# Kernel tuning notes

Measured on AMD Instinct MI355X. Metric: run time of the kernel, lower is better.

Reference implementation:

```python
import jax, jax.numpy as jnp
import numpy as np

DIM = 2560; HEADS = 20; HEAD_DIM = 128
N_EXP = 4; TOP_K = 2; HID = 6912; SHID = 3584
B = 1; S = 2048
EPS = 1e-6


def setup_inputs():
    key = jax.random.key(0)
    ks = jax.random.split(key, 16)
    r = lambda i, shape, s=0.02: jax.random.normal(ks[i], shape, jnp.float32) * s
    # rope as [1,S,1,HD/2,2,2] rotation matrices: [[cos,-sin],[sin,cos]]
    ang = jax.random.uniform(ks[0], (1, S, 1, HEAD_DIM // 2), jnp.float32) * (2.0 * np.pi)
    c, s_ = jnp.cos(ang), jnp.sin(ang)
    rope = jnp.stack([jnp.stack([c, -s_], -1), jnp.stack([s_, c], -1)], -2)
    return dict(
        hidden_states=jax.random.normal(ks[1], (B, S, DIM), jnp.float32),
        temb=jax.random.normal(ks[2], (B, DIM), jnp.float32),
        rope=rope,
        adaln_w=r(3, (6 * DIM, DIM)), adaln_b=jnp.zeros((6 * DIM,), jnp.float32),
        qkv_w=r(4, (3 * DIM, DIM)), qkv_b=jnp.zeros((3 * DIM,), jnp.float32),
        qn_w=jnp.ones((DIM,), jnp.float32), kn_w=jnp.ones((DIM,), jnp.float32),
        out_w=r(5, (DIM, DIM)), out_b=jnp.zeros((DIM,), jnp.float32),
        gate_w=r(6, (N_EXP, DIM), 1.0 / DIM ** 0.5),
        ew1=r(7, (N_EXP, HID, DIM)), ew2=r(8, (N_EXP, DIM, HID)), ew3=r(9, (N_EXP, HID, DIM)),
        sw1=r(10, (SHID, DIM)), sw2=r(11, (DIM, SHID)), sw3=r(12, (SHID, DIM)),
    )


def _layernorm(x):  # elementwise_affine=False, eps=1e-6
    m = x.mean(-1, keepdims=True)
    v = ((x - m) ** 2).mean(-1, keepdims=True)
    return (x - m) * jax.lax.rsqrt(v + EPS)


def _rmsnorm(x, w):  # DistributedRMSNorm, tp_size=1
    return x * jax.lax.rsqrt((x ** 2).mean(-1, keepdims=True) + EPS) * w


def _apply_rope(x, rope):  # x:[B,S,H,D], rope:[1,S,1,D/2,2,2]
    b, s, h, d = x.shape
    x_ = x.reshape(b, s, h, d // 2, 1, 2)
    out = rope[..., 0] * x_[..., 0] + rope[..., 1] * x_[..., 1]  # [B,S,H,D/2,2]
    return out.reshape(b, s, h, d)


def _swiglu(x, w1, w2, w3):
    return (jax.nn.silu(x @ w1.T) * (x @ w3.T)) @ w2.T


def _forward(hidden_states, temb, rope, adaln_w, adaln_b, qkv_w, qkv_b, qn_w, kn_w,
             out_w, out_b, gate_w, ew1, ew2, ew3, sw1, sw2, sw3):
    b, s, d = hidden_states.shape
    # adaLN modulation: SiLU -> Linear -> [:, None] -> chunk(6)
    mod = (jax.nn.silu(temb) @ adaln_w.T + adaln_b)[:, None, :]
    shift_msa, scale_msa, gate_msa, shift_mlp, scale_mlp, gate_mlp = jnp.split(mod, 6, axis=-1)
    # --- attention ---
    nh = _layernorm(hidden_states) * (1.0 + scale_msa) + shift_msa
    qkv = nh @ qkv_w.T + qkv_b
    q, k, v = jnp.split(qkv, 3, axis=-1)  # each [B,S,inner_dim]
    q = _rmsnorm(q, qn_w)  # RMS over full inner_dim (all heads)
    k = _rmsnorm(k, kn_w)
    q = q.reshape(b, s, HEADS, HEAD_DIM)
    k = k.reshape(b, s, HEADS, HEAD_DIM)
    v = v.reshape(b, s, HEADS, HEAD_DIM)
    q = _apply_rope(q, rope)
    k = _apply_rope(k, rope)
    attn = jnp.einsum('bqhd,bkhd->bhqk', q, k) * (HEAD_DIM ** -0.5)
    attn = jax.nn.softmax(attn, axis=-1)
    o = jnp.einsum('bhqk,bkhd->bqhd', attn, v).reshape(b, s, HEADS * HEAD_DIM)
    o = o @ out_w.T + out_b
    hidden_states = gate_msa * o + hidden_states
    # --- MoE SwiGLU feed-forward ---
    nh = _layernorm(hidden_states) * (1.0 + scale_mlp) + shift_mlp
    x = nh.reshape(-1, d)  # [T,d]
    scores = jax.nn.softmax(x @ gate_w.T, axis=-1)  # [T,E]
    tw, ti = jax.lax.top_k(scores, TOP_K)  # norm_topk_prob=False
    t = x.shape[0]
    wdense = jnp.zeros((t, N_EXP), x.dtype).at[jnp.arange(t)[:, None], ti].set(tw)
    y = jnp.zeros_like(x)
    for e in range(N_EXP):  # fixed small expert count
        y = y + wdense[:, e:e + 1] * _swiglu(x, ew1[e], ew2[e], ew3[e])
    y = y.reshape(b, s, d) + _swiglu(nh, sw1, sw2, sw3)  # shared experts on identity
    return gate_mlp * y + hidden_states


def reference(hidden_states, temb, rope, adaln_w, adaln_b, qkv_w, qkv_b, qn_w, kn_w,
              out_w, out_b, gate_w, ew1, ew2, ew3, sw1, sw2, sw3):
    return _forward(hidden_states, temb, rope, adaln_w, adaln_b, qkv_w, qkv_b, qn_w, kn_w,
                    out_w, out_b, gate_w, ew1, ew2, ew3, sw1, sw2, sw3)
```

## Files before the change

### kernel.cpp

```cpp
#include <hip/hip_runtime.h>

#define DIM 2560
#define T_TOK 2048
#define NHEADS 20
#define HD 128
#define HID_E 6912
#define SHID_E 3584
#define MPAD 5120

typedef _Float16 f16x8 __attribute__((ext_vector_type(8)));
typedef float f32x4 __attribute__((ext_vector_type(4)));
typedef unsigned short u16x8 __attribute__((ext_vector_type(8)));

#define MFMA16(a, b, c) __builtin_amdgcn_mfma_f32_16x16x32_f16((a), (b), (c), 0, 0, 0)

__device__ inline unsigned short f2h(float f) {
  return __builtin_bit_cast(unsigned short, (_Float16)f);
}
__device__ inline float h2f(unsigned short u) {
  return (float)__builtin_bit_cast(_Float16, u);
}
__device__ inline float wave_sum(float v) {
#pragma unroll
  for (int off = 32; off > 0; off >>= 1) v += __shfl_down(v, off, 64);
  return v;
}
__device__ inline void gld16(const void* g, void* l) {
  __builtin_amdgcn_global_load_lds((const __attribute__((address_space(1))) void*)g,
                                   (__attribute__((address_space(3))) void*)l, 16, 0, 0);
}


__global__ __launch_bounds__(256) void silu_k(const float* __restrict__ t,
                                              float* __restrict__ ss) {
  int i = blockIdx.x * 256 + threadIdx.x;
  if (i < DIM) {
    float v = t[i];
    ss[i] = v / (1.f + expf(-v));
  }
}

__global__ __launch_bounds__(256) void cvt_f16(const float* __restrict__ in,
                                               unsigned short* __restrict__ outp, int n8) {
  const int stride = gridDim.x * 256;
  for (int i = blockIdx.x * 256 + threadIdx.x; i < n8; i += stride) {
    float4 a = *(const float4*)(in + (size_t)i * 8);
    float4 b = *(const float4*)(in + (size_t)i * 8 + 4);
    u16x8 u;
    u[0] = f2h(a.x); u[1] = f2h(a.y); u[2] = f2h(a.z); u[3] = f2h(a.w);
    u[4] = f2h(b.x); u[5] = f2h(b.y); u[6] = f2h(b.z); u[7] = f2h(b.w);
    *(u16x8*)&outp[(size_t)i * 8] = u;
  }
}

__global__ __launch_bounds__(256) void cvt_pair(const float* __restrict__ w1,
                                                const float* __restrict__ w3,
                                                unsigned short* __restrict__ outp) {
  const int j = blockIdx.x;
  const int g = j >> 5, r = j & 31;
  const float* src = (r < 16) ? (w1 + (size_t)(g * 16 + r) * DIM)
                              : (w3 + (size_t)(g * 16 + (r & 15)) * DIM);
  unsigned short* dst = outp + (size_t)j * DIM;
  for (int i = threadIdx.x; i < 320; i += 256) {
    float4 a = *(const float4*)(src + i * 8);
    float4 b = *(const float4*)(src + i * 8 + 4);
    u16x8 u;
    u[0] = f2h(a.x); u[1] = f2h(a.y); u[2] = f2h(a.z); u[3] = f2h(a.w);
    u[4] = f2h(b.x); u[5] = f2h(b.y); u[6] = f2h(b.z); u[7] = f2h(b.w);
    *(u16x8*)&dst[i * 8] = u;
  }
}

__global__ __launch_bounds__(256) void adaln_gemv(const float* __restrict__ ss,
                                                  const float* __restrict__ W,
                                                  const float* __restrict__ bias,
                                                  float* __restrict__ mod) {
  const int lane = threadIdx.x & 63;
  const int j = blockIdx.x * 4 + (threadIdx.x >> 6);
  const float* wr = W + (size_t)j * DIM;
  float p = 0.f;
  for (int i = lane; i < 640; i += 64) {
    float4 w = *(const float4*)(wr + i * 4);
    float4 x = *(const float4*)(ss + i * 4);
    p += w.x * x.x + w.y * x.y + w.z * x.z + w.w * x.w;
  }
  p = wave_sum(p);
  if (lane == 0) mod[j] = p + bias[j];
}

__global__ __launch_bounds__(256) void ln_mod(const float* __restrict__ x,
                                              const float* __restrict__ shift,
                                              const float* __restrict__ scale,
                                              unsigned short* __restrict__ outp) {
  __shared__ float rbuf[8];
  const int t = blockIdx.x, tid = threadIdx.x, lane = tid & 63, wid = tid >> 6;
  const float* xr = x + (size_t)t * DIM;
  float s = 0.f, sq = 0.f;
  for (int i = tid; i < 640; i += 256) {
    float4 v = *(const float4*)(xr + i * 4);
    s += v.x + v.y + v.z + v.w;
    sq += v.x * v.x + v.y * v.y + v.z * v.z + v.w * v.w;
  }
  s = wave_sum(s);
  sq = wave_sum(sq);
  if (lane == 0) {
    rbuf[wid] = s;
    rbuf[4 + wid] = sq;
  }
  __syncthreads();
  float S = rbuf[0] + rbuf[1] + rbuf[2] + rbuf[3];
  float SQ = rbuf[4] + rbuf[5] + rbuf[6] + rbuf[7];
  float mean = S * (1.f / DIM);
  float rs = rsqrtf(SQ * (1.f / DIM) - mean * mean + 1e-6f);
  for (int i = tid; i < 640; i += 256) {
    float4 v = *(const float4*)(xr + i * 4);
    float4 sc4 = *(const float4*)(scale + i * 4);
    float4 sh4 = *(const float4*)(shift + i * 4);
    ushort4 u;
    u.x = f2h((v.x - mean) * rs * (1.f + sc4.x) + sh4.x);
    u.y = f2h((v.y - mean) * rs * (1.f + sc4.y) + sh4.y);
    u.z = f2h((v.z - mean) * rs * (1.f + sc4.z) + sh4.z);
    u.w = f2h((v.w - mean) * rs * (1.f + sc4.w) + sh4.w);
    *(ushort4*)&outp[(size_t)t * DIM + i * 4] = u;
  }
}

__global__ __launch_bounds__(256) void rmsrope(const unsigned short* __restrict__ qkv,
                                               const float* __restrict__ qn,
                                               const float* __restrict__ kn,
                                               const float* __restrict__ rope,
                                               unsigned short* __restrict__ qh,
                                               unsigned short* __restrict__ kh) {
  __shared__ float rbuf[8];
  const int t = blockIdx.x, tid = threadIdx.x, lane = tid & 63, wid = tid >> 6;
  const unsigned short* row = qkv + (size_t)t * 7680;
  float sq = 0.f, sk = 0.f;
  for (int i = tid; i < 320; i += 256) {
    f16x8 qv = *(const f16x8*)(row + i * 8);
    f16x8 kv = *(const f16x8*)(row + DIM + i * 8);
#pragma unroll
    for (int j = 0; j < 8; ++j) {
      float q = (float)qv[j], k = (float)kv[j];
      sq += q * q;
      sk += k * k;
    }
  }
  sq = wave_sum(sq);
  sk = wave_sum(sk);
  if (lane == 0) {
    rbuf[wid] = sq;
    rbuf[4 + wid] = sk;
  }
  __syncthreads();
  float SQ = rbuf[0] + rbuf[1] + rbuf[2] + rbuf[3];
  float SK = rbuf[4] + rbuf[5] + rbuf[6] + rbuf[7];
  float rq = rsqrtf(SQ * (1.f / DIM) + 1e-6f) * 0.08838834764831845f;
  float rk = rsqrtf(SK * (1.f / DIM) + 1e-6f);
  for (int pp = tid; pp < 1280; pp += 256) {
    int c = pp * 2;
    float qe = h2f(row[c]) * rq * qn[c], qo = h2f(row[c + 1]) * rq * qn[c + 1];
    float ke = h2f(row[DIM + c]) * rk * kn[c], ko = h2f(row[DIM + c + 1]) * rk * kn[c + 1];
    float4 rr = *(const float4*)(rope + (size_t)t * 256 + (pp & 63) * 4);
    unsigned qp = (unsigned)f2h(rr.x * qe + rr.y * qo) |
                  ((unsigned)f2h(rr.z * qe + rr.w * qo) << 16);
    unsigned kp = (unsigned)f2h(rr.x * ke + rr.y * ko) |
                  ((unsigned)f2h(rr.z * ke + rr.w * ko) << 16);
    *(unsigned*)&qh[(size_t)t * DIM + c] = qp;
    *(unsigned*)&kh[(size_t)t * DIM + c] = kp;
  }
}

__global__ void transpose_v(const unsigned short* __restrict__ in,
                            unsigned short* __restrict__ outp) {
  __shared__ unsigned short tile[32][33];
  const int bx = blockIdx.x * 32;
  const int by = blockIdx.y * 32;
  const int tx = threadIdx.x, ty = threadIdx.y;
  for (int j = ty; j < 32; j += 8)
    tile[j][tx] = in[(size_t)(by + j) * 7680 + 5120 + bx + tx];
  __syncthreads();
  for (int j = ty; j < 32; j += 8)
    outp[(size_t)(bx + j) * T_TOK + by + tx] = tile[tx][j];
}

__global__ __launch_bounds__(256) void fattn(const unsigned short* __restrict__ qh,
                                             const unsigned short* __restrict__ kh,
                                             const unsigned short* __restrict__ vt,
                                             unsigned short* __restrict__ obuf) {
  __shared__ unsigned short sK[64 * 128];
  __shared__ unsigned short sV[128 * 64];
  __shared__ unsigned short sP[64 * 64];
  __shared__ float sRedM[4][64];
  __shared__ float sRedL[4][64];
  __shared__ float sM[64];
  __shared__ float sL[64];
  const int tid = threadIdx.x, lane = tid & 63, wv = tid >> 6;
  const int g = lane >> 4, fr = lane & 15;
  const int h = blockIdx.y;
  const int q0 = blockIdx.x * 64;

  {
    const int r = tid >> 2, qt = tid & 3;
    const unsigned short* gp = qh + (size_t)(q0 + r) * DIM + h * HD + qt * 32;
    uint4 v0 = ((const uint4*)gp)[0];
    uint4 v1 = ((const uint4*)gp)[1];
    uint4 v2 = ((const uint4*)gp)[2];
    uint4 v3 = ((const uint4*)gp)[3];
    unsigned short* dst = &sK[r * 128];
    const int cb = qt * 4, rs = r & 15;
    *(uint4*)&dst[((cb + 0) ^ rs) * 8] = v0;
    *(uint4*)&dst[((cb + 1) ^ rs) * 8] = v1;
    *(uint4*)&dst[((cb + 2) ^ rs) * 8] = v2;
    *(uint4*)&dst[((cb + 3) ^ rs) * 8] = v3;
  }
  __syncthreads();
  f16x8 qfrag[4][4];
#pragma unroll
  for (int ni = 0; ni < 4; ++ni) {
#pragma unroll
    for (int kt = 0; kt < 4; ++kt) {
      int r = ni * 16 + fr;
      qfrag[ni][kt] = *(const f16x8*)&sK[r * 128 + (((kt * 4 + g) ^ (r & 15)) << 3)];
    }
  }
  __syncthreads();

  f32x4 acco[4][2];
  f32x4 mprev[4];
  float mrun[4], lrun[4];
#pragma unroll
  for (int i = 0; i < 4; ++i) {
    acco[i][0] = (f32x4)0.f;
    acco[i][1] = (f32x4)0.f;
    mprev[i] = (f32x4)(-1e30f);
    mrun[i] = -1e30f;
    lrun[i] = 0.f;
  }

  for (int kt0 = 0; kt0 < T_TOK; kt0 += 64) {
    {
      const int r = tid >> 2, qt = tid & 3;
      const unsigned short* gp = kh + (size_t)(kt0 + r) * DIM + h * HD + qt * 32;
      uint4 v0 = ((const uint4*)gp)[0];
      uint4 v1 = ((const uint4*)gp)[1];
      uint4 v2 = ((const uint4*)gp)[2];
      uint4 v3 = ((const uint4*)gp)[3];
      unsigned short* dst = &sK[r * 128];
      const int cb = qt * 4, rs = r & 15;
      *(uint4*)&dst[((cb + 0) ^ rs) * 8] = v0;
      *(uint4*)&dst[((cb + 1) ^ rs) * 8] = v1;
      *(uint4*)&dst[((cb + 2) ^ rs) * 8] = v2;
      *(uint4*)&dst[((cb + 3) ^ rs) * 8] = v3;
      const int rv = tid >> 1, hf = tid & 1;
      const unsigned short* gv = vt + (size_t)(h * HD + rv) * T_TOK + kt0 + hf * 32;
      uint4 w0 = ((const uint4*)gv)[0];
      uint4 w1 = ((const uint4*)gv)[1];
      uint4 w2 = ((const uint4*)gv)[2];
      uint4 w3 = ((const uint4*)gv)[3];
      unsigned short* dv = &sV[rv * 64];
      const int cv = hf * 4, rvs = rv & 7;
      *(uint4*)&dv[((cv + 0) ^ rvs) * 8] = w0;
      *(uint4*)&dv[((cv + 1) ^ rvs) * 8] = w1;
      *(uint4*)&dv[((cv + 2) ^ rvs) * 8] = w2;
      *(uint4*)&dv[((cv + 3) ^ rvs) * 8] = w3;
    }
    __syncthreads();

    f32x4 accs[4] = {(f32x4)0.f, (f32x4)0.f, (f32x4)0.f, (f32x4)0.f};
#pragma unroll
    for (int kt = 0; kt < 4; ++kt) {
      int r = wv * 16 + fr;
      f16x8 ak = *(const f16x8*)&sK[r * 128 + (((kt * 4 + g) ^ (r & 15)) << 3)];
#pragma unroll
      for (int ni = 0; ni < 4; ++ni) accs[ni] = MFMA16(ak, qfrag[ni][kt], accs[ni]);
    }

    float pm[4];
#pragma unroll
    for (int ni = 0; ni < 4; ++ni) {
      float m = fmaxf(fmaxf(accs[ni][0], accs[ni][1]), fmaxf(accs[ni][2], accs[ni][3]));
      m = fmaxf(m, __shfl_xor(m, 16));
      m = fmaxf(m, __shfl_xor(m, 32));
      pm[ni] = m;
    }
    if (g == 0) {
#pragma unroll
      for (int ni = 0; ni < 4; ++ni) sRedM[wv][ni * 16 + fr] = pm[ni];
    }
    __syncthreads();
    float mnew[4];
#pragma unroll
    for (int ni = 0; ni < 4; ++ni) {
      int q = ni * 16 + fr;
      float mt = fmaxf(fmaxf(sRedM[0][q], sRedM[1][q]), fmaxf(sRedM[2][q], sRedM[3][q]));
      mnew[ni] = fmaxf(mrun[ni], mt);
    }
    float lsum[4];
#pragma unroll
    for (int ni = 0; ni < 4; ++ni) {
      float l0 = 0.f;
#pragma unroll
      for (int i = 0; i < 4; ++i) {
        float p = __expf(accs[ni][i] - mnew[ni]);
        accs[ni][i] = p;
        l0 += p;
      }
      l0 += __shfl_xor(l0, 16);
      l0 += __shfl_xor(l0, 32);
      lsum[ni] = l0;
    }
    if (g == 0) {
#pragma unroll
      for (int ni = 0; ni < 4; ++ni) sRedL[wv][ni * 16 + fr] = lsum[ni];
      if (wv == 0) {
#pragma unroll
        for (int ni = 0; ni < 4; ++ni) sM[ni * 16 + fr] = mnew[ni];
      }
    }
#pragma unroll
    for (int ni = 0; ni < 4; ++ni) {
      int q = ni * 16 + fr;
      unsigned p01 = (unsigned)f2h(accs[ni][0]) | ((unsigned)f2h(accs[ni][1]) << 16);
      unsigned p23 = (unsigned)f2h(accs[ni][2]) | ((unsigned)f2h(accs[ni][3]) << 16);
      uint2 pk;
      pk.x = p01;
      pk.y = p23;
      *(uint2*)&sP[q * 64 + ((((wv << 1) | (g >> 1)) ^ (q & 7)) << 3) + ((g & 1) << 2)] = pk;
    }
    __syncthreads();
#pragma unroll
    for (int ni = 0; ni < 4; ++ni) {
      int q = ni * 16 + fr;
      float lt = sRedL[0][q] + sRedL[1][q] + sRedL[2][q] + sRedL[3][q];
      lrun[ni] = lrun[ni] * __expf(mrun[ni] - mnew[ni]) + lt;
      mrun[ni] = mnew[ni];
    }

#pragma unroll
    for (int mi = 0; mi < 4; ++mi) {
      f32x4 mn = *(const f32x4*)&sM[mi * 16 + g * 4];
      f32x4 sc;
#pragma unroll
      for (int i = 0; i < 4; ++i) sc[i] = __expf(mprev[mi][i] - mn[i]);
      acco[mi][0] *= sc;
      acco[mi][1] *= sc;
      mprev[mi] = mn;
    }
#pragma unroll
    for (int ktp = 0; ktp < 2; ++ktp) {
      f16x8 bv[2];
#pragma unroll
      for (int nd = 0; nd < 2; ++nd) {
        int r = wv * 32 + nd * 16 + fr;
        bv[nd] = *(const f16x8*)&sV[r * 64 + (((ktp * 4 + g) ^ (r & 7)) << 3)];
      }
#pragma unroll
      for (int mi = 0; mi < 4; ++mi) {
        int r = mi * 16 + fr;
        f16x8 ap = *(const f16x8*)&sP[r * 64 + (((ktp * 4 + g) ^ (r & 7)) << 3)];
        acco[mi][0] = MFMA16(ap, bv[0], acco[mi][0]);
        acco[mi][1] = MFMA16(ap, bv[1], acco[mi][1]);
      }
    }
    __syncthreads();
  }

  if (wv == 0 && g == 0) {
#pragma unroll
    for (int ni = 0; ni < 4; ++ni) sL[ni * 16 + fr] = 1.f / lrun[ni];
  }
  __syncthreads();
#pragma unroll
  for (int mi = 0; mi < 4; ++mi) {
    f32x4 li = *(const f32x4*)&sL[mi * 16 + g * 4];
#pragma unroll
    for (int nd = 0; nd < 2; ++nd) {
#pragma unroll
      for (int i = 0; i < 4; ++i) {
        float o = acco[mi][nd][i] * li[i];
        obuf[(size_t)(q0 + mi * 16 + g * 4 + i) * DIM + h * HD + wv * 32 + nd * 16 + fr] =
            f2h(o);
      }
    }
  }
}

__global__ __launch_bounds__(256) void ln2_route(const float* __restrict__ x,
                                                 const float* __restrict__ shift,
                                                 const float* __restrict__ scale,
                                                 const float* __restrict__ gw,
                                                 unsigned short* __restrict__ nh2,
                                                 float* __restrict__ wd) {
  __shared__ float rbuf[8];
  __shared__ float gbuf[4][4];
  const int t = blockIdx.x, tid = threadIdx.x, lane = tid & 63, wid = tid >> 6;
  const float* xr = x + (size_t)t * DIM;
  float s = 0.f, sq = 0.f;
  for (int i = tid; i < 640; i += 256) {
    float4 v = *(const float4*)(xr + i * 4);
    s += v.x + v.y + v.z + v.w;
    sq += v.x * v.x + v.y * v.y + v.z * v.z + v.w * v.w;
  }
  s = wave_sum(s);
  sq = wave_sum(sq);
  if (lane == 0) {
    rbuf[wid] = s;
    rbuf[4 + wid] = sq;
  }
  __syncthreads();
  float S = rbuf[0] + rbuf[1] + rbuf[2] + rbuf[3];
  float SQ = rbuf[4] + rbuf[5] + rbuf[6] + rbuf[7];
  float mean = S * (1.f / DIM);
  float rs = rsqrtf(SQ * (1.f / DIM) - mean * mean + 1e-6f);
  float g0 = 0.f, g1 = 0.f, g2 = 0.f, g3 = 0.f;
  for (int i = tid; i < 640; i += 256) {
    float4 v = *(const float4*)(xr + i * 4);
    float4 sc4 = *(const float4*)(scale + i * 4);
    float4 sh4 = *(const float4*)(shift + i * 4);
    float y0 = (v.x - mean) * rs * (1.f + sc4.x) + sh4.x;
    float y1 = (v.y - mean) * rs * (1.f + sc4.y) + sh4.y;
    float y2 = (v.z - mean) * rs * (1.f + sc4.z) + sh4.z;
    float y3 = (v.w - mean) * rs * (1.f + sc4.w) + sh4.w;
    ushort4 u;
    u.x = f2h(y0); u.y = f2h(y1); u.z = f2h(y2); u.w = f2h(y3);
    *(ushort4*)&nh2[(size_t)t * DIM + i * 4] = u;
    float4 w0 = *(const float4*)(gw + i * 4);
    float4 w1 = *(const float4*)(gw + DIM + i * 4);
    float4 w2 = *(const float4*)(gw + 2 * DIM + i * 4);
    float4 w3 = *(const float4*)(gw + 3 * DIM + i * 4);
    g0 += y0 * w0.x + y1 * w0.y + y2 * w0.z + y3 * w0.w;
    g1 += y0 * w1.x + y1 * w1.y + y2 * w1.z + y3 * w1.w;
    g2 += y0 * w2.x + y1 * w2.y + y2 * w2.z + y3 * w2.w;
    g3 += y0 * w3.x + y1 * w3.y + y2 * w3.z + y3 * w3.w;
  }
  g0 = wave_sum(g0);
  g1 = wave_sum(g1);
  g2 = wave_sum(g2);
  g3 = wave_sum(g3);
  if (lane == 0) {
    gbuf[wid][0] = g0; gbuf[wid][1] = g1; gbuf[wid][2] = g2; gbuf[wid][3] = g3;
  }
  __syncthreads();
  if (tid == 0) {
    float l[4];
#pragma unroll
    for (int e = 0; e < 4; ++e) l[e] = gbuf[0][e] + gbuf[1][e] + gbuf[2][e] + gbuf[3][e];
    float mx = fmaxf(fmaxf(l[0], l[1]), fmaxf(l[2], l[3]));
    float ex[4], sum = 0.f;
#pragma unroll
    for (int e = 0; e < 4; ++e) { ex[e] = expf(l[e] - mx); sum += ex[e]; }
    float p[4];
#pragma unroll
    for (int e = 0; e < 4; ++e) p[e] = ex[e] / sum;
    int i1 = 0;
    for (int e = 1; e < 4; ++e)
      if (p[e] > p[i1]) i1 = e;
    int i2 = -1;
    for (int e = 0; e < 4; ++e) {
      if (e == i1) continue;
      if (i2 < 0 || p[e] > p[i2]) i2 = e;
    }
    float w[4] = {0.f, 0.f, 0.f, 0.f};
    w[i1] = p[i1];
    w[i2] = p[i2];
    *(float4*)&wd[(size_t)t * 4] = make_float4(w[0], w[1], w[2], w[3]);
  }
}

__global__ __launch_bounds__(256) void route_compact(const float* __restrict__ wd,
                                                     int* __restrict__ idx_all,
                                                     int* __restrict__ seg,
                                                     int* __restrict__ slotAB,
                                                     float* __restrict__ wAB) {
  __shared__ unsigned short c[256][4];
  __shared__ int offs[256][4];
  __shared__ int segs[5];
  const int t = threadIdx.x;
  for (int i = t; i < MPAD; i += 256) idx_all[i] = 0;
  unsigned char sel[8];
  float wv4[8][4];
  unsigned short lc[4] = {0, 0, 0, 0};
#pragma unroll
  for (int k = 0; k < 8; ++k) {
    int tok = t * 8 + k;
    float4 w = *(const float4*)&wd[(size_t)tok * 4];
    wv4[k][0] = w.x; wv4[k][1] = w.y; wv4[k][2] = w.z; wv4[k][3] = w.w;
    unsigned m = 0;
    if (w.x != 0.f) { m |= 1; lc[0]++; }
    if (w.y != 0.f) { m |= 2; lc[1]++; }
    if (w.z != 0.f) { m |= 4; lc[2]++; }
    if (w.w != 0.f) { m |= 8; lc[3]++; }
    sel[k] = (unsigned char)m;
  }
#pragma unroll
  for (int e = 0; e < 4; ++e) c[t][e] = lc[e];
  __syncthreads();
  if (t == 0) {
    int run[4] = {0, 0, 0, 0};
    for (int i = 0; i < 256; ++i) {
#pragma unroll
      for (int e = 0; e < 4; ++e) {
        offs[i][e] = run[e];
        run[e] += c[i][e];
      }
    }
    int s = 0;
    segs[0] = 0;
#pragma unroll
    for (int e = 0; e < 4; ++e) {
      s += (run[e] + 255) & ~255;
      segs[e + 1] = s;
    }
#pragma unroll
    for (int e = 0; e < 5; ++e) seg[e] = segs[e];
  }
  __syncthreads();
  int o[4];
#pragma unroll
  for (int e = 0; e < 4; ++e) o[e] = segs[e] + offs[t][e];
#pragma unroll
  for (int k = 0; k < 8; ++k) {
    int tok = t * 8 + k;
    unsigned m = sel[k];
    int sl[2] = {0, 0};
    float sw[2] = {0.f, 0.f};
    int ns = 0;
#pragma unroll
    for (int e = 0; e < 4; ++e) {
      if ((m >> e) & 1) {
        if (ns < 2) { sl[ns] = o[e]; sw[ns] = wv4[k][e]; }
        idx_all[o[e]++] = tok;
        ns++;
      }
    }
    if (ns == 1) { sl[1] = sl[0]; sw[1] = 0.f; }
    slotAB[tok * 2] = sl[0];
    slotAB[tok * 2 + 1] = sl[1];
    wAB[tok * 2] = sw[0];
    wAB[tok * 2 + 1] = sw[1];
  }
}

template <int EPI, int MODE>
__global__ __launch_bounds__(256) void gemm128(
    const unsigned short* __restrict__ A, const unsigned short* __restrict__ B,
    const float* __restrict__ bias, void* __restrict__ Cv,
    const float* __restrict__ aux0, const float* __restrict__ aux1,
    const int* __restrict__ idx, const int* __restrict__ seg,
    const int* __restrict__ slotAB, const float* __restrict__ wAB,
    const unsigned short* __restrict__ yc, int M, int N, int K) {
  __shared__ unsigned short smem[16384];
  const int tid = threadIdx.x;
  const int lane = tid & 63;
  const int wv = tid >> 6;
  const int nwg = gridDim.x;
  const int bid = blockIdx.x;
  const int swzb = (bid & 7) * (nwg >> 3) + (bid >> 3);
  const int gm = M >> 7;
  const int m0 = (swzb % gm) * 128, n0 = (swzb / gm) * 128;
  if (MODE != 0 && m0 >= seg[4]) return;

  const unsigned short* Bp = B;
  if constexpr (MODE != 0) {
    int e = 0;
#pragma unroll
    for (int i = 1; i < 4; ++i)
      if (m0 >= seg[i]) e = i;
    Bp = B + (size_t)e * N * K;
  }

  const int wm = (wv >> 1) * 64, wn = (wv & 1) * 64;
  const int fr = lane & 15, fc = lane >> 4;

  const int rl = lane >> 2, ch = lane & 3;
  const int R1 = wv * 16 + rl;
  const int R2 = 64 + R1;
  const int co1 = ((ch ^ ((R1 >> 1) & 3)) << 3);
  const int co2 = ((ch ^ ((R2 >> 1) & 3)) << 3);
  const size_t ar1 = (size_t)(m0 + R1) * K;
  const size_t ar2 = (size_t)(m0 + R2) * K;
  const unsigned short* gA1 = A + ar1 + co1;
  const unsigned short* gA2 = A + ar2 + co2;
  const unsigned short* gB1 = Bp + (size_t)(n0 + R1) * K + co1;
  const unsigned short* gB2 = Bp + (size_t)(n0 + R2) * K + co2;
  const int lA1 = (wv * 16) * 32, lA2 = (64 + wv * 16) * 32;

  f32x4 acc[4][4];
#pragma unroll
  for (int i = 0; i < 4; ++i) {
#pragma unroll
    for (int j = 0; j < 4; ++j) acc[i][j] = (f32x4)0.f;
  }

  auto STAGE = [&](int buf, int kt) {
    unsigned short* base = smem + buf * 8192;
    gld16(gA1 + kt, base + lA1);
    gld16(gA2 + kt, base + lA2);
    gld16(gB1 + kt, base + 4096 + lA1);
    gld16(gB2 + kt, base + 4096 + lA2);
  };
  auto COMPUTE = [&](int buf) {
    const unsigned short* sA = smem + buf * 8192;
    const unsigned short* sB = sA + 4096;
    f16x8 a[4], b[4];
#pragma unroll
    for (int mi = 0; mi < 4; ++mi) {
      int r = wm + mi * 16 + fr;
      a[mi] = *(const f16x8*)&sA[r * 32 + ((fc ^ ((r >> 1) & 3)) << 3)];
    }
#pragma unroll
    for (int ni = 0; ni < 4; ++ni) {
      int r = wn + ni * 16 + fr;
      b[ni] = *(const f16x8*)&sB[r * 32 + ((fc ^ ((r >> 1) & 3)) << 3)];
    }
#pragma unroll
    for (int mi = 0; mi < 4; ++mi) {
#pragma unroll
      for (int ni = 0; ni < 4; ++ni) acc[mi][ni] = MFMA16(a[mi], b[ni], acc[mi][ni]);
    }
  };

  const int nk = K >> 5;
  STAGE(0, 0);
  __syncthreads();
  int cur = 0;
  for (int t = 1; t < nk; ++t) {
    STAGE(cur ^ 1, t << 5);
    COMPUTE(cur);
    __syncthreads();
    cur ^= 1;
  }
  COMPUTE(cur);

#pragma unroll
  for (int mi = 0; mi < 4; ++mi) {
#pragma unroll
    for (int ni = 0; ni < 4; ++ni) {
      const int n = n0 + wn + ni * 16 + fr;
      const int mb = m0 + wm + mi * 16 + fc * 4;
#pragma unroll
      for (int i = 0; i < 4; ++i) {
        const int m = mb + i;
        float v = acc[mi][ni][i];
        const size_t cidx = (size_t)m * N + n;
        if constexpr (EPI == 1) {
          ((float*)Cv)[cidx] = aux0[n] * (v + bias[n]) + aux1[cidx];
        } else if constexpr (EPI == 4) {
          if (bias) v += bias[n];
          ((unsigned short*)Cv)[cidx] = f2h(v);
        } else if constexpr (EPI == 6) {
          const int sA_ = slotAB[m * 2], sB_ = slotAB[m * 2 + 1];
          const float wA_ = wAB[m * 2], wB_ = wAB[m * 2 + 1];
          float vm = wA_ * h2f(yc[(size_t)sA_ * N + n]) + wB_ * h2f(yc[(size_t)sB_ * N + n]);
          ((float*)Cv)[cidx] = aux0[n] * (v + vm) + aux1[cidx];
        }
      }
    }
  }
}

template <int EPI, int MODE>
__global__ __launch_bounds__(512) void gemm256(
    const unsigned short* __restrict__ A, const unsigned short* __restrict__ B,
    const float* __restrict__ bias, void* __restrict__ Cv,
    const int* __restrict__ idx, const int* __restrict__ seg,
    int M, int N, int K) {
  __shared__ unsigned short smem[49152];
  const int tid = threadIdx.x;
  const int lane = tid & 63;
  const int wv = tid >> 6;
  const int wr = wv >> 2;
  const int wc = wv & 3;
  const int fr = lane & 15, fc = lane >> 4;

  const int nwg = gridDim.x;
  const int bid = blockIdx.x;
  const int swzb = (bid & 7) * (nwg >> 3) + (bid >> 3);
  const int gm = M >> 8;
  const int m0 = (swzb % gm) * 256, n0 = (swzb / gm) * 256;
  if (MODE != 0 && m0 >= seg[4]) return;

  const unsigned short* Bp = B;
  if constexpr (MODE != 0) {
    int e = 0;
#pragma unroll
    for (int i = 1; i < 4; ++i)
      if (m0 >= seg[i]) e = i;
    Bp = B + (size_t)e * N * K;
  }

  const int srow = (lane >> 2);
  const int srcc = ((lane & 3) ^ ((lane >> 3) & 3)) << 3;
  int mr0, mr1;
  if constexpr (MODE == 1) {
    mr0 = idx[m0 + wv * 16 + srow];
    mr1 = idx[m0 + 128 + wv * 16 + srow];
  } else {
    mr0 = m0 + wv * 16 + srow;
    mr1 = m0 + 128 + wv * 16 + srow;
  }
  const unsigned short* gA0 = A + (size_t)mr0 * K + srcc;
  const unsigned short* gA1 = A + (size_t)mr1 * K + srcc;
  const unsigned short* gB0 = Bp + (size_t)(n0 + wv * 16 + srow) * K + srcc;
  const unsigned short* gB1 = Bp + (size_t)(n0 + 128 + wv * 16 + srow) * K + srcc;
  const int lw = wv << 9;

  const int sw = (fr >> 1) & 3;
  const int fo = ((fc ^ sw) << 3);
  const int aoff = (wr * 128 + fr) * 32 + fo;
  const int boff = (wc * 64 + fr) * 32 + fo;

  f32x4 acc[8][4];
#pragma unroll
  for (int i = 0; i < 8; ++i) {
#pragma unroll
    for (int j = 0; j < 4; ++j) acc[i][j] = (f32x4)0.f;
  }

  const int nk = K >> 5;
  gld16(gA0, &smem[lw]);
  gld16(gA1, &smem[4096 + lw]);
  gld16(gB0, &smem[8192 + lw]);
  gld16(gB1, &smem[12288 + lw]);
  gld16(gA0 + 32, &smem[16384 + lw]);
  gld16(gA1 + 32, &smem[16384 + 4096 + lw]);
  gld16(gB0 + 32, &smem[16384 + 8192 + lw]);
  gld16(gB1 + 32, &smem[16384 + 12288 + lw]);

  int cur = 0;
  for (int t = 0; t < nk; ++t) {
    if (t < nk - 1)
      asm volatile("s_waitcnt vmcnt(4)" ::: "memory");
    else
      asm volatile("s_waitcnt vmcnt(0)" ::: "memory");
    __builtin_amdgcn_s_barrier();
    __builtin_amdgcn_sched_barrier(0);

    const unsigned short* sA = smem + cur * 16384;
    const unsigned short* sB = sA + 8192;
    int nxt = cur + 2;
    if (nxt >= 3) nxt -= 3;
    unsigned short* nbase = smem + nxt * 16384;
    const bool more = (t + 2) < nk;
    const int kn = (t + 2) << 5;

    f16x8 b0 = *(const f16x8*)&sB[boff];
    f16x8 b1 = *(const f16x8*)&sB[boff + 512];
    f16x8 b2 = *(const f16x8*)&sB[boff + 1024];
    f16x8 b3 = *(const f16x8*)&sB[boff + 1536];
    f16x8 a0 = *(const f16x8*)&sA[aoff];
    f16x8 a1 = *(const f16x8*)&sA[aoff + 512];
    f16x8 a2 = *(const f16x8*)&sA[aoff + 1024];
    f16x8 a3 = *(const f16x8*)&sA[aoff + 1536];
    f16x8 a4 = *(const f16x8*)&sA[aoff + 2048];
    f16x8 a5 = *(const f16x8*)&sA[aoff + 2560];
    f16x8 a6 = *(const f16x8*)&sA[aoff + 3072];
    f16x8 a7 = *(const f16x8*)&sA[aoff + 3584];
    __builtin_amdgcn_sched_barrier(0);
    if (more) {
      gld16(gA0 + kn, nbase + lw);
      gld16(gA1 + kn, nbase + 4096 + lw);
      gld16(gB0 + kn, nbase + 8192 + lw);
      gld16(gB1 + kn, nbase + 12288 + lw);
    }
    __builtin_amdgcn_sched_barrier(0);
    acc[0][0] = MFMA16(a0, b0, acc[0][0]);
    acc[0][1] = MFMA16(a0, b1, acc[0][1]);
    acc[0][2] = MFMA16(a0, b2, acc[0][2]);
    acc[0][3] = MFMA16(a0, b3, acc[0][3]);
    acc[1][0] = MFMA16(a1, b0, acc[1][0]);
    acc[1][1] = MFMA16(a1, b1, acc[1][1]);
    acc[1][2] = MFMA16(a1, b2, acc[1][2]);
    acc[1][3] = MFMA16(a1, b3, acc[1][3]);
    acc[2][0] = MFMA16(a2, b0, acc[2][0]);
    acc[2][1] = MFMA16(a2, b1, acc[2][1]);
    acc[2][2] = MFMA16(a2, b2, acc[2][2]);
    acc[2][3] = MFMA16(a2, b3, acc[2][3]);
    acc[3][0] = MFMA16(a3, b0, acc[3][0]);
    acc[3][1] = MFMA16(a3, b1, acc[3][1]);
    acc[3][2] = MFMA16(a3, b2, acc[3][2]);
    acc[3][3] = MFMA16(a3, b3, acc[3][3]);
    acc[4][0] = MFMA16(a4, b0, acc[4][0]);
    acc[4][1] = MFMA16(a4, b1, acc[4][1]);
    acc[4][2] = MFMA16(a4, b2, acc[4][2]);
    acc[4][3] = MFMA16(a4, b3, acc[4][3]);
    acc[5][0] = MFMA16(a5, b0, acc[5][0]);
    acc[5][1] = MFMA16(a5, b1, acc[5][1]);
    acc[5][2] = MFMA16(a5, b2, acc[5][2]);
    acc[5][3] = MFMA16(a5, b3, acc[5][3]);
    acc[6][0] = MFMA16(a6, b0, acc[6][0]);
    acc[6][1] = MFMA16(a6, b1, acc[6][1]);
    acc[6][2] = MFMA16(a6, b2, acc[6][2]);
    acc[6][3] = MFMA16(a6, b3, acc[6][3]);
    acc[7][0] = MFMA16(a7, b0, acc[7][0]);
    acc[7][1] = MFMA16(a7, b1, acc[7][1]);
    acc[7][2] = MFMA16(a7, b2, acc[7][2]);
    acc[7][3] = MFMA16(a7, b3, acc[7][3]);

    cur += 1;
    if (cur >= 3) cur -= 3;
  }

  if constexpr (EPI == 5) {
    unsigned short* Ch = (unsigned short*)Cv;
    const int Nh = N >> 1;
#pragma unroll
    for (int mi = 0; mi < 8; ++mi) {
#pragma unroll
      for (int p = 0; p < 2; ++p) {
        const int hcol = (((n0 + wc * 64) >> 5) + p) * 16 + fr;
        const int mb = m0 + wr * 128 + mi * 16 + fc * 4;
#pragma unroll
        for (int i = 0; i < 4; ++i) {
          const int m = mb + i;
          float v1 = acc[mi][2 * p][i];
          float v3 = acc[mi][2 * p + 1][i];
          float y = v1 / (1.f + __expf(-v1)) * v3;
          Ch[(size_t)m * Nh + hcol] = f2h(y);
        }
      }
    }
  } else {
    unsigned short* Ch = (unsigned short*)Cv;
#pragma unroll
    for (int mi = 0; mi < 8; ++mi) {
#pragma unroll
      for (int ni = 0; ni < 4; ++ni) {
        const int n = n0 + wc * 64 + ni * 16 + fr;
        const int mb = m0 + wr * 128 + mi * 16 + fc * 4;
#pragma unroll
        for (int i = 0; i < 4; ++i) {
          const int m = mb + i;
          float v = acc[mi][ni][i];
          if (bias) v += bias[n];
          Ch[(size_t)m * N + n] = f2h(v);
        }
      }
    }
  }
}


extern "C" void kernel_launch(void* const* d_in, const int* in_sizes, int n_in,
                              void* d_out, int out_size, void* d_ws, size_t ws_size,
                              hipStream_t stream) {
  (void)in_sizes; (void)n_in; (void)out_size; (void)ws_size;
  const float* hs = (const float*)d_in[0];
  const float* temb = (const float*)d_in[1];
  const float* rope = (const float*)d_in[2];
  const float* adaw = (const float*)d_in[3];
  const float* adab = (const float*)d_in[4];
  const float* qkvw = (const float*)d_in[5];
  const float* qkvb = (const float*)d_in[6];
  const float* qnw = (const float*)d_in[7];
  const float* knw = (const float*)d_in[8];
  const float* outw = (const float*)d_in[9];
  const float* outb = (const float*)d_in[10];
  const float* gatew = (const float*)d_in[11];
  const float* ew1 = (const float*)d_in[12];
  const float* ew2 = (const float*)d_in[13];
  const float* ew3 = (const float*)d_in[14];
  const float* sw1 = (const float*)d_in[15];
  const float* sw2 = (const float*)d_in[16];
  const float* sw3 = (const float*)d_in[17];
  float* out = (float*)d_out;
  char* ws = (char*)d_ws;

  size_t off = 0;
  auto give = [&](size_t nbytes) {
    size_t r = off;
    off += (nbytes + 255) & ~(size_t)255;
    return r;
  };
  const size_t T = T_TOK, D = DIM;
  size_t o_mod = give(15360 * 4);
  size_t o_ss = give(D * 4);
  size_t o_wd = give(T * 4 * 4);
  size_t o_idx = give(MPAD * 4);
  size_t o_seg = give(8 * 4);
  size_t o_slot = give(T * 2 * 4);
  size_t o_wab = give(T * 2 * 4);
  size_t o_nh = give(T * D * 2);
  size_t o_qkvh = give(T * 7680 * 2);
  size_t o_qh = give(T * D * 2);
  size_t o_kh = give(T * D * 2);
  size_t o_vt = give(T * D * 2);
  size_t o_obf = give(T * D * 2);
  size_t o_h2 = give(T * D * 4);
  size_t o_yc = give((size_t)MPAD * D * 2);
  size_t o_hmid2 = give(T * SHID_E * 2);
  size_t o_qkvw = give((size_t)7680 * 2560 * 2);
  size_t o_outw = give((size_t)2560 * 2560 * 2);
  size_t o_ewA = give((size_t)4 * 2 * HID_E * 2560 * 2);
  size_t o_ew2 = give((size_t)4 * 2560 * HID_E * 2);
  size_t o_swA = give((size_t)2 * SHID_E * 2560 * 2);
  size_t o_sw2 = give((size_t)2560 * SHID_E * 2);

  float* mod = (float*)(ws + o_mod);
  float* ss = (float*)(ws + o_ss);
  float* wd = (float*)(ws + o_wd);
  int* idxb = (int*)(ws + o_idx);
  int* segp = (int*)(ws + o_seg);
  int* slotAB = (int*)(ws + o_slot);
  float* wAB = (float*)(ws + o_wab);
  unsigned short* nh_h = (unsigned short*)(ws + o_nh);
  unsigned short* qkvh = (unsigned short*)(ws + o_qkvh);
  unsigned short* qh = (unsigned short*)(ws + o_qh);
  unsigned short* kh = (unsigned short*)(ws + o_kh);
  unsigned short* vt = (unsigned short*)(ws + o_vt);
  unsigned short* obf = (unsigned short*)(ws + o_obf);
  float* h2 = (float*)(ws + o_h2);
  unsigned short* yc = (unsigned short*)(ws + o_yc);
  unsigned short* hmid2 = (unsigned short*)(ws + o_hmid2);
  unsigned short* qkvw_h = (unsigned short*)(ws + o_qkvw);
  unsigned short* outw_h = (unsigned short*)(ws + o_outw);
  unsigned short* ewA_h = (unsigned short*)(ws + o_ewA);
  unsigned short* ew2_h = (unsigned short*)(ws + o_ew2);
  unsigned short* swA_h = (unsigned short*)(ws + o_swA);
  unsigned short* sw2_h = (unsigned short*)(ws + o_sw2);
  unsigned short* nh2 = nh_h;
  unsigned short* hmid = qkvh;

  cvt_f16<<<2048, 256, 0, stream>>>(qkvw, qkvw_h, 7680 * 2560 / 8);
  cvt_f16<<<2048, 256, 0, stream>>>(outw, outw_h, 2560 * 2560 / 8);
  cvt_f16<<<2048, 256, 0, stream>>>(ew2, ew2_h, 4 * 2560 * HID_E / 8);
  cvt_f16<<<2048, 256, 0, stream>>>(sw2, sw2_h, 2560 * SHID_E / 8);
  for (int e = 0; e < 4; ++e) {
    cvt_pair<<<2 * HID_E, 256, 0, stream>>>(ew1 + (size_t)e * HID_E * DIM,
                                            ew3 + (size_t)e * HID_E * DIM,
                                            ewA_h + (size_t)e * 2 * HID_E * DIM);
  }
  cvt_pair<<<2 * SHID_E, 256, 0, stream>>>(sw1, sw3, swA_h);
  silu_k<<<10, 256, 0, stream>>>(temb, ss);
  adaln_gemv<<<3840, 256, 0, stream>>>(ss, adaw, adab, mod);
  ln_mod<<<T, 256, 0, stream>>>(hs, mod, mod + D, nh_h);
  gemm256<4, 0><<<240, 512, 0, stream>>>(nh_h, qkvw_h, qkvb, qkvh,
                                         nullptr, nullptr, 2048, 7680, 2560);
  rmsrope<<<T, 256, 0, stream>>>(qkvh, qnw, knw, rope, qh, kh);
  transpose_v<<<dim3(80, 64), dim3(32, 8), 0, stream>>>(qkvh, vt);
  fattn<<<dim3(32, 20), 256, 0, stream>>>(qh, kh, vt, obf);
  gemm128<1, 0><<<16 * 20, 256, 0, stream>>>(obf, outw_h, outb, h2,
                                             mod + 2 * D, hs, nullptr, nullptr,
                                             nullptr, nullptr, nullptr, 2048, 2560, 2560);
  ln2_route<<<T, 256, 0, stream>>>(h2, mod + 3 * D, mod + 4 * D, gatew, nh2, wd);
  route_compact<<<1, 256, 0, stream>>>(wd, idxb, segp, slotAB, wAB);
  gemm256<5, 1><<<20 * 54, 512, 0, stream>>>(nh2, ewA_h, nullptr, hmid,
                                             idxb, segp, MPAD, 2 * HID_E, 2560);
  gemm256<4, 2><<<20 * 10, 512, 0, stream>>>(hmid, ew2_h, nullptr, yc,
                                             nullptr, segp, MPAD, 2560, 6912);
  gemm256<5, 0><<<8 * 28, 512, 0, stream>>>(nh2, swA_h, nullptr, hmid2,
                                            nullptr, nullptr, 2048, 2 * SHID_E, 2560);
  gemm128<6, 0><<<16 * 20, 256, 0, stream>>>(hmid2, sw2_h, nullptr, out,
                                             mod + 5 * D, h2, nullptr, nullptr,
                                             slotAB, wAB, yc, 2048, 2560, 3584);
}
```

Before: 1.401 ms.

## Merge weight-conversion launches, process two query tiles per attention block, raise MFMA priority

```diff
diff --git a/kernel.cpp b/kernel.cpp
--- a/kernel.cpp
+++ b/kernel.cpp
@@ -40,27 +40,53 @@
   }
 }
 
-__global__ __launch_bounds__(256) void cvt_f16(const float* __restrict__ in,
-                                               unsigned short* __restrict__ outp, int n8) {
-  const int stride = gridDim.x * 256;
-  for (int i = blockIdx.x * 256 + threadIdx.x; i < n8; i += stride) {
-    float4 a = *(const float4*)(in + (size_t)i * 8);
-    float4 b = *(const float4*)(in + (size_t)i * 8 + 4);
+__global__ __launch_bounds__(256) void cvt_all4(
+    const float* __restrict__ s0, unsigned short* __restrict__ d0, long n0,
+    const float* __restrict__ s1, unsigned short* __restrict__ d1, long n1,
+    const float* __restrict__ s2, unsigned short* __restrict__ d2, long n2,
+    const float* __restrict__ s3, unsigned short* __restrict__ d3, long n3) {
+  const long stride = (long)gridDim.x * 256;
+  const long t01 = n0 + n1, t012 = t01 + n2, tot = t012 + n3;
+  for (long i = (long)blockIdx.x * 256 + threadIdx.x; i < tot; i += stride) {
+    const float* s;
+    unsigned short* d;
+    long j;
+    if (i < n0) { s = s0; d = d0; j = i; }
+    else if (i < t01) { s = s1; d = d1; j = i - n0; }
+    else if (i < t012) { s = s2; d = d2; j = i - t01; }
+    else { s = s3; d = d3; j = i - t012; }
+    float4 a = *(const float4*)(s + j * 8);
+    float4 b = *(const float4*)(s + j * 8 + 4);
     u16x8 u;
     u[0] = f2h(a.x); u[1] = f2h(a.y); u[2] = f2h(a.z); u[3] = f2h(a.w);
     u[4] = f2h(b.x); u[5] = f2h(b.y); u[6] = f2h(b.z); u[7] = f2h(b.w);
-    *(u16x8*)&outp[(size_t)i * 8] = u;
-  }
-}
-
-__global__ __launch_bounds__(256) void cvt_pair(const float* __restrict__ w1,
-                                                const float* __restrict__ w3,
-                                                unsigned short* __restrict__ outp) {
+    *(u16x8*)&d[j * 8] = u;
+  }
+}
+
+__global__ __launch_bounds__(256) void cvt_pair_all(
+    const float* __restrict__ ew1, const float* __restrict__ ew3,
+    const float* __restrict__ sw1, const float* __restrict__ sw3,
+    unsigned short* __restrict__ ewA, unsigned short* __restrict__ swA) {
   const int j = blockIdx.x;
-  const int g = j >> 5, r = j & 31;
+  const float *w1, *w3;
+  unsigned short* dst;
+  int row;
+  if (j < 4 * 2 * HID_E) {
+    const int e = j / (2 * HID_E);
+    row = j - e * 2 * HID_E;
+    w1 = ew1 + (size_t)e * HID_E * DIM;
+    w3 = ew3 + (size_t)e * HID_E * DIM;
+    dst = ewA + (size_t)e * 2 * HID_E * DIM + (size_t)row * DIM;
+  } else {
+    row = j - 4 * 2 * HID_E;
+    w1 = sw1;
+    w3 = sw3;
+    dst = swA + (size_t)row * DIM;
+  }
+  const int g = row >> 5, r = row & 31;
   const float* src = (r < 16) ? (w1 + (size_t)(g * 16 + r) * DIM)
                               : (w3 + (size_t)(g * 16 + (r & 15)) * DIM);
-  unsigned short* dst = outp + (size_t)j * DIM;
   for (int i = threadIdx.x; i < 320; i += 256) {
     float4 a = *(const float4*)(src + i * 8);
     float4 b = *(const float4*)(src + i * 8 + 4);
@@ -188,6 +214,7 @@
                                              const unsigned short* __restrict__ vt,
                                              unsigned short* __restrict__ obuf) {
   __shared__ unsigned short sK[64 * 128];
+  __shared__ unsigned short sQb[64 * 128];
   __shared__ unsigned short sV[128 * 64];
   __shared__ unsigned short sP[64 * 64];
   __shared__ float sRedM[4][64];
@@ -197,44 +224,61 @@
   const int tid = threadIdx.x, lane = tid & 63, wv = tid >> 6;
   const int g = lane >> 4, fr = lane & 15;
   const int h = blockIdx.y;
-  const int q0 = blockIdx.x * 64;
+  const int q0 = blockIdx.x * 128;
 
   {
     const int r = tid >> 2, qt = tid & 3;
-    const unsigned short* gp = qh + (size_t)(q0 + r) * DIM + h * HD + qt * 32;
-    uint4 v0 = ((const uint4*)gp)[0];
-    uint4 v1 = ((const uint4*)gp)[1];
-    uint4 v2 = ((const uint4*)gp)[2];
-    uint4 v3 = ((const uint4*)gp)[3];
-    unsigned short* dst = &sK[r * 128];
     const int cb = qt * 4, rs = r & 15;
-    *(uint4*)&dst[((cb + 0) ^ rs) * 8] = v0;
-    *(uint4*)&dst[((cb + 1) ^ rs) * 8] = v1;
-    *(uint4*)&dst[((cb + 2) ^ rs) * 8] = v2;
-    *(uint4*)&dst[((cb + 3) ^ rs) * 8] = v3;
+    {
+      const unsigned short* gp = qh + (size_t)(q0 + r) * DIM + h * HD + qt * 32;
+      uint4 v0 = ((const uint4*)gp)[0];
+      uint4 v1 = ((const uint4*)gp)[1];
+      uint4 v2 = ((const uint4*)gp)[2];
+      uint4 v3 = ((const uint4*)gp)[3];
+      unsigned short* dst = &sK[r * 128];
+      *(uint4*)&dst[((cb + 0) ^ rs) * 8] = v0;
+      *(uint4*)&dst[((cb + 1) ^ rs) * 8] = v1;
+      *(uint4*)&dst[((cb + 2) ^ rs) * 8] = v2;
+      *(uint4*)&dst[((cb + 3) ^ rs) * 8] = v3;
+    }
+    {
+      const unsigned short* gp = qh + (size_t)(q0 + 64 + r) * DIM + h * HD + qt * 32;
+      uint4 v0 = ((const uint4*)gp)[0];
+      uint4 v1 = ((const uint4*)gp)[1];
+      uint4 v2 = ((const uint4*)gp)[2];
+      uint4 v3 = ((const uint4*)gp)[3];
+      unsigned short* dst = &sQb[r * 128];
+      *(uint4*)&dst[((cb + 0) ^ rs) * 8] = v0;
+      *(uint4*)&dst[((cb + 1) ^ rs) * 8] = v1;
+      *(uint4*)&dst[((cb + 2) ^ rs) * 8] = v2;
+      *(uint4*)&dst[((cb + 3) ^ rs) * 8] = v3;
+    }
   }
   __syncthreads();
-  f16x8 qfrag[4][4];
+  f16x8 qfragA[4][4];
 #pragma unroll
   for (int ni = 0; ni < 4; ++ni) {
 #pragma unroll
     for (int kt = 0; kt < 4; ++kt) {
       int r = ni * 16 + fr;
-      qfrag[ni][kt] = *(const f16x8*)&sK[r * 128 + (((kt * 4 + g) ^ (r & 15)) << 3)];
+      qfragA[ni][kt] = *(const f16x8*)&sK[r * 128 + (((kt * 4 + g) ^ (r & 15)) << 3)];
     }
   }
   __syncthreads();
 
-  f32x4 acco[4][2];
-  f32x4 mprev[4];
-  float mrun[4], lrun[4];
-#pragma unroll
-  for (int i = 0; i < 4; ++i) {
-    acco[i][0] = (f32x4)0.f;
-    acco[i][1] = (f32x4)0.f;
-    mprev[i] = (f32x4)(-1e30f);
-    mrun[i] = -1e30f;
-    lrun[i] = 0.f;
+  f32x4 acco[2][4][2];
+  f32x4 mprev[2][4];
+  float mrun[2][4], lrun[2][4];
+#pragma unroll
+  for (int s = 0; s < 2; ++s) {
+#pragma unroll
+    for (int i = 0; i < 4; ++i) {
+      acco[s][i][0] = (f32x4)0.f;
+      acco[s][i][1] = (f32x4)0.f;
+      mprev[s][i] = (f32x4)(-1e30f);
+      mrun[s][i] = -1e30f;
+      lrun[s][i] = 0.f;
+    }
   }
 
   for (int kt0 = 0; kt0 < T_TOK; kt0 += 64) {
@@ -266,122 +310,138 @@
     }
     __syncthreads();
 
-    f32x4 accs[4] = {(f32x4)0.f, (f32x4)0.f, (f32x4)0.f, (f32x4)0.f};
-#pragma unroll
-    for (int kt = 0; kt < 4; ++kt) {
-      int r = wv * 16 + fr;
-      f16x8 ak = *(const f16x8*)&sK[r * 128 + (((kt * 4 + g) ^ (r & 15)) << 3)];
-#pragma unroll
-      for (int ni = 0; ni < 4; ++ni) accs[ni] = MFMA16(ak, qfrag[ni][kt], accs[ni]);
-    }
-
-    float pm[4];
-#pragma unroll
-    for (int ni = 0; ni < 4; ++ni) {
-      float m = fmaxf(fmaxf(accs[ni][0], accs[ni][1]), fmaxf(accs[ni][2], accs[ni][3]));
-      m = fmaxf(m, __shfl_xor(m, 16));
-      m = fmaxf(m, __shfl_xor(m, 32));
-      pm[ni] = m;
-    }
-    if (g == 0) {
-#pragma unroll
-      for (int ni = 0; ni < 4; ++ni) sRedM[wv][ni * 16 + fr] = pm[ni];
+#pragma unroll
+    for (int s = 0; s < 2; ++s) {
+      f32x4 accs[4] = {(f32x4)0.f, (f32x4)0.f, (f32x4)0.f, (f32x4)0.f};
+#pragma unroll
+      for (int kt = 0; kt < 4; ++kt) {
+        int r = wv * 16 + fr;
+        f16x8 ak = *(const f16x8*)&sK[r * 128 + (((kt * 4 + g) ^ (r & 15)) << 3)];
+#pragma unroll
+        for (int ni = 0; ni < 4; ++ni) {
+          f16x8 q;
+          if (s == 0) {
+            q = qfragA[ni][kt];
+          } else {
+            int rq = ni * 16 + fr;
+            q = *(const f16x8*)&sQb[rq * 128 + (((kt * 4 + g) ^ (rq & 15)) << 3)];
+          }
+          accs[ni] = MFMA16(ak, q, accs[ni]);
+        }
+      }
+
+      float pm[4];
+#pragma unroll
+      for (int ni = 0; ni < 4; ++ni) {
+        float m = fmaxf(fmaxf(accs[ni][0], accs[ni][1]), fmaxf(accs[ni][2], accs[ni][3]));
+        m = fmaxf(m, __shfl_xor(m, 16));
+        m = fmaxf(m, __shfl_xor(m, 32));
+        pm[ni] = m;
+      }
+      if (g == 0) {
+#pragma unroll
+        for (int ni = 0; ni < 4; ++ni) sRedM[wv][ni * 16 + fr] = pm[ni];
+      }
+      __syncthreads();
+      float mnew[4];
+#pragma unroll
+      for (int ni = 0; ni < 4; ++ni) {
+        int q = ni * 16 + fr;
+        float mt = fmaxf(fmaxf(sRedM[0][q], sRedM[1][q]), fmaxf(sRedM[2][q], sRedM[3][q]));
+        mnew[ni] = fmaxf(mrun[s][ni], mt);
+      }
+      float lsum[4];
+#pragma unroll
+      for (int ni = 0; ni < 4; ++ni) {
+        float l0 = 0.f;
+#pragma unroll
+        for (int i = 0; i < 4; ++i) {
+          float p = __expf(accs[ni][i] - mnew[ni]);
+          accs[ni][i] = p;
+          l0 += p;
+        }
+        l0 += __shfl_xor(l0, 16);
+        l0 += __shfl_xor(l0, 32);
+        lsum[ni] = l0;
+      }
+      if (g == 0) {
+#pragma unroll
+        for (int ni = 0; ni < 4; ++ni) sRedL[wv][ni * 16 + fr] = lsum[ni];
+        if (wv == 0) {
+#pragma unroll
+          for (int ni = 0; ni < 4; ++ni) sM[ni * 16 + fr] = mnew[ni];
+        }
+      }
+#pragma unroll
+      for (int ni = 0; ni < 4; ++ni) {
+        int q = ni * 16 + fr;
+        unsigned p01 = (unsigned)f2h(accs[ni][0]) | ((unsigned)f2h(accs[ni][1]) << 16);
+        unsigned p23 = (unsigned)f2h(accs[ni][2]) | ((unsigned)f2h(accs[ni][3]) << 16);
+        uint2 pk;
+        pk.x = p01;
+        pk.y = p23;
+        *(uint2*)&sP[q * 64 + ((((wv << 1) | (g >> 1)) ^ (q & 7)) << 3) + ((g & 1) << 2)] = pk;
+      }
+      __syncthreads();
+#pragma unroll
+      for (int ni = 0; ni < 4; ++ni) {
+        int q = ni * 16 + fr;
+        float lt = sRedL[0][q] + sRedL[1][q] + sRedL[2][q] + sRedL[3][q];
+        lrun[s][ni] = lrun[s][ni] * __expf(mrun[s][ni] - mnew[ni]) + lt;
+        mrun[s][ni] = mnew[ni];
+      }
+
+#pragma unroll
+      for (int mi = 0; mi < 4; ++mi) {
+        f32x4 mn = *(const f32x4*)&sM[mi * 16 + g * 4];
+        f32x4 sc;
+#pragma unroll
+        for (int i = 0; i < 4; ++i) sc[i] = __expf(mprev[s][mi][i] - mn[i]);
+        acco[s][mi][0] *= sc;
+        acco[s][mi][1] *= sc;
+        mprev[s][mi] = mn;
+      }
+#pragma unroll
+      for (int ktp = 0; ktp < 2; ++ktp) {
+        f16x8 bv[2];
+#pragma unroll
+        for (int nd = 0; nd < 2; ++nd) {
+          int r = wv * 32 + nd * 16 + fr;
+          bv[nd] = *(const f16x8*)&sV[r * 64 + (((ktp * 4 + g) ^ (r & 7)) << 3)];
+        }
+#pragma unroll
+        for (int mi = 0; mi < 4; ++mi) {
+          int r = mi * 16 + fr;
+          f16x8 ap = *(const f16x8*)&sP[r * 64 + (((ktp * 4 + g) ^ (r & 7)) << 3)];
+          acco[s][mi][0] = MFMA16(ap, bv[0], acco[s][mi][0]);
+          acco[s][mi][1] = MFMA16(ap, bv[1], acco[s][mi][1]);
+        }
+      }
+      __syncthreads();
+    }
+  }
+
+#pragma unroll
+  for (int s = 0; s < 2; ++s) {
+    if (wv == 0 && g == 0) {
+#pragma unroll
+      for (int ni = 0; ni < 4; ++ni) sL[ni * 16 + fr] = 1.f / lrun[s][ni];
     }
     __syncthreads();
-    float mnew[4];
-#pragma unroll
-    for (int ni = 0; ni < 4; ++ni) {
-      int q = ni * 16 + fr;
-      float mt = fmaxf(fmaxf(sRedM[0][q], sRedM[1][q]), fmaxf(sRedM[2][q], sRedM[3][q]));
-      mnew[ni] = fmaxf(mrun[ni], mt);
-    }
-    float lsum[4];
-#pragma unroll
-    for (int ni = 0; ni < 4; ++ni) {
-      float l0 = 0.f;
-#pragma unroll
-      for (int i = 0; i < 4; ++i) {
-        float p = __expf(accs[ni][i] - mnew[ni]);
-        accs[ni][i] = p;
-        l0 += p;
-      }
-      l0 += __shfl_xor(l0, 16);
-      l0 += __shfl_xor(l0, 32);
-      lsum[ni] = l0;
-    }
-    if (g == 0) {
-#pragma unroll
-      for (int ni = 0; ni < 4; ++ni) sRedL[wv][ni * 16 + fr] = lsum[ni];
-      if (wv == 0) {
-#pragma unroll
-        for (int ni = 0; ni < 4; ++ni) sM[ni * 16 + fr] = mnew[ni];
-      }
-    }
-#pragma unroll
-    for (int ni = 0; ni < 4; ++ni) {
-      int q = ni * 16 + fr;
-      unsigned p01 = (unsigned)f2h(accs[ni][0]) | ((unsigned)f2h(accs[ni][1]) << 16);
-      unsigned p23 = (unsigned)f2h(accs[ni][2]) | ((unsigned)f2h(accs[ni][3]) << 16);
-      uint2 pk;
-      pk.x = p01;
-      pk.y = p23;
-      *(uint2*)&sP[q * 64 + ((((wv << 1) | (g >> 1)) ^ (q & 7)) << 3) + ((g & 1) << 2)] = pk;
+#pragma unroll
+    for (int mi = 0; mi < 4; ++mi) {
+      f32x4 li = *(const f32x4*)&sL[mi * 16 + g * 4];
+#pragma unroll
+      for (int nd = 0; nd < 2; ++nd) {
+#pragma unroll
+        for (int i = 0; i < 4; ++i) {
+          float o = acco[s][mi][nd][i] * li[i];
+          obuf[(size_t)(q0 + s * 64 + mi * 16 + g * 4 + i) * DIM + h * HD + wv * 32 +
+               nd * 16 + fr] = f2h(o);
+        }
+      }
     }
     __syncthreads();
-#pragma unroll
-    for (int ni = 0; ni < 4; ++ni) {
-      int q = ni * 16 + fr;
-      float lt = sRedL[0][q] + sRedL[1][q] + sRedL[2][q] + sRedL[3][q];
-      lrun[ni] = lrun[ni] * __expf(mrun[ni] - mnew[ni]) + lt;
-      mrun[ni] = mnew[ni];
-    }
-
-#pragma unroll
-    for (int mi = 0; mi < 4; ++mi) {
-      f32x4 mn = *(const f32x4*)&sM[mi * 16 + g * 4];
-      f32x4 sc;
-#pragma unroll
-      for (int i = 0; i < 4; ++i) sc[i] = __expf(mprev[mi][i] - mn[i]);
-      acco[mi][0] *= sc;
-      acco[mi][1] *= sc;
-      mprev[mi] = mn;
-    }
-#pragma unroll
-    for (int ktp = 0; ktp < 2; ++ktp) {
-      f16x8 bv[2];
-#pragma unroll
-      for (int nd = 0; nd < 2; ++nd) {
-        int r = wv * 32 + nd * 16 + fr;
-        bv[nd] = *(const f16x8*)&sV[r * 64 + (((ktp * 4 + g) ^ (r & 7)) << 3)];
-      }
-#pragma unroll
-      for (int mi = 0; mi < 4; ++mi) {
-        int r = mi * 16 + fr;
-        f16x8 ap = *(const f16x8*)&sP[r * 64 + (((ktp * 4 + g) ^ (r & 7)) << 3)];
-        acco[mi][0] = MFMA16(ap, bv[0], acco[mi][0]);
-        acco[mi][1] = MFMA16(ap, bv[1], acco[mi][1]);
-      }
-    }
-    __syncthreads();
-  }
-
-  if (wv == 0 && g == 0) {
-#pragma unroll
-    for (int ni = 0; ni < 4; ++ni) sL[ni * 16 + fr] = 1.f / lrun[ni];
-  }
-  __syncthreads();
-#pragma unroll
-  for (int mi = 0; mi < 4; ++mi) {
-    f32x4 li = *(const f32x4*)&sL[mi * 16 + g * 4];
-#pragma unroll
-    for (int nd = 0; nd < 2; ++nd) {
-#pragma unroll
-      for (int i = 0; i < 4; ++i) {
-        float o = acco[mi][nd][i] * li[i];
-        obuf[(size_t)(q0 + mi * 16 + g * 4 + i) * DIM + h * HD + wv * 32 + nd * 16 + fr] =
-            f2h(o);
-      }
-    }
   }
 }
 
@@ -764,6 +824,7 @@
       gld16(gB1 + kn, nbase + 12288 + lw);
     }
     __builtin_amdgcn_sched_barrier(0);
+    __builtin_amdgcn_s_setprio(1);
     acc[0][0] = MFMA16(a0, b0, acc[0][0]);
     acc[0][1] = MFMA16(a0, b1, acc[0][1]);
     acc[0][2] = MFMA16(a0, b2, acc[0][2]);
@@ -796,6 +857,7 @@
     acc[7][1] = MFMA16(a7, b1, acc[7][1]);
     acc[7][2] = MFMA16(a7, b2, acc[7][2]);
     acc[7][3] = MFMA16(a7, b3, acc[7][3]);
+    __builtin_amdgcn_s_setprio(0);
 
     cur += 1;
     if (cur >= 3) cur -= 3;
@@ -921,16 +983,12 @@
   unsigned short* nh2 = nh_h;
   unsigned short* hmid = qkvh;
 
-  cvt_f16<<<2048, 256, 0, stream>>>(qkvw, qkvw_h, 7680 * 2560 / 8);
-  cvt_f16<<<2048, 256, 0, stream>>>(outw, outw_h, 2560 * 2560 / 8);
-  cvt_f16<<<2048, 256, 0, stream>>>(ew2, ew2_h, 4 * 2560 * HID_E / 8);
-  cvt_f16<<<2048, 256, 0, stream>>>(sw2, sw2_h, 2560 * SHID_E / 8);
-  for (int e = 0; e < 4; ++e) {
-    cvt_pair<<<2 * HID_E, 256, 0, stream>>>(ew1 + (size_t)e * HID_E * DIM,
-                                            ew3 + (size_t)e * HID_E * DIM,
-                                            ewA_h + (size_t)e * 2 * HID_E * DIM);
-  }
-  cvt_pair<<<2 * SHID_E, 256, 0, stream>>>(sw1, sw3, swA_h);
+  cvt_all4<<<4096, 256, 0, stream>>>(qkvw, qkvw_h, 7680L * 2560 / 8,
+                                     outw, outw_h, 2560L * 2560 / 8,
+                                     ew2, ew2_h, 4L * 2560 * HID_E / 8,
+                                     sw2, sw2_h, 2560L * SHID_E / 8);
+  cvt_pair_all<<<4 * 2 * HID_E + 2 * SHID_E, 256, 0, stream>>>(ew1, ew3, sw1, sw3,
+                                                               ewA_h, swA_h);
   silu_k<<<10, 256, 0, stream>>>(temb, ss);
   adaln_gemv<<<3840, 256, 0, stream>>>(ss, adaw, adab, mod);
   ln_mod<<<T, 256, 0, stream>>>(hs, mod, mod + D, nh_h);
@@ -938,7 +996,7 @@
                                          nullptr, nullptr, 2048, 7680, 2560);
   rmsrope<<<T, 256, 0, stream>>>(qkvh, qnw, knw, rope, qh, kh);
   transpose_v<<<dim3(80, 64), dim3(32, 8), 0, stream>>>(qkvh, vt);
-  fattn<<<dim3(32, 20), 256, 0, stream>>>(qh, kh, vt, obf);
+  fattn<<<dim3(16, 20), 256, 0, stream>>>(qh, kh, vt, obf);
   gemm128<1, 0><<<16 * 20, 256, 0, stream>>>(obf, outw_h, outb, h2,
                                              mod + 2 * D, hs, nullptr, nullptr,
                                              nullptr, nullptr, nullptr, 2048, 2560, 2560);
```

Result: slower. 1.526 ms (+8.9%).
